# Optimization experiments

Measured on AMD Instinct MI355X. Metric: run time of the kernel, lower is better.

Reference implementation:

```python
import jax, jax.numpy as jnp
import numpy as np
import math

B, T, M, C, H = 2, 2048, 77, 512, 8
D = C // H  # head dim = 64


def setup_inputs() -> dict:
    key = jax.random.key(0)
    ks = jax.random.split(key, 20)
    s = 0.02
    inp = {
        "x": jax.random.normal(ks[0], (B, T, C), jnp.float32),
        "c": jax.random.normal(ks[1], (B, M, C), jnp.float32),
        # causal mask for self-attention (masked_fill where == 0)
        "attn_mask": jnp.tril(jnp.ones((T, T), jnp.int32))[None, None],
        "padding_mask": jnp.ones((B, M), jnp.int32),
    }
    names = ["Wq", "Wk", "Wv", "Wkc", "Wvc", "Wg1", "Wg2", "Wp"]
    for i, n in enumerate(names):
        inp[n] = jax.random.normal(ks[2 + i], (C, C), jnp.float32) * s
        inp["b" + n[1:]] = jnp.zeros((C,), jnp.float32)
    return inp


def _heads(t):
    # [B, S, C] -> [B, S, H, D]
    return t.reshape(t.shape[0], t.shape[1], H, D)


def reference(x, c, attn_mask, padding_mask,
              Wq, bq, Wk, bk, Wv, bv, Wkc, bkc, Wvc, bvc,
              Wg1, bg1, Wg2, bg2, Wp, bp):
    scale = 1.0 / math.sqrt(D)
    q = _heads(x @ Wq + bq)      # [B,T,H,D]
    k = _heads(x @ Wk + bk)      # [B,T,H,D]
    v = _heads(x @ Wv + bv)
    k_c = _heads(c @ Wkc + bkc)  # [B,M,H,D]
    v_c = _heads(c @ Wvc + bvc)

    # self-attention branch
    att = jnp.einsum("bthd,bshd->bhts", q, k) * scale   # [B,H,T,T]
    att = jnp.where(attn_mask == 0, -jnp.inf, att)
    att = jax.nn.softmax(att, axis=-1)
    y = jnp.einsum("bhts,bshd->bthd", att, v).reshape(B, T, C)

    # cross-attention branch to condition c
    att_c = jnp.einsum("bthd,bmhd->bhtm", q, k_c) * scale  # [B,H,T,M]
    att_c = jnp.where(padding_mask[:, None, None, :] == 0, -jnp.inf, att_c)
    att_c = jax.nn.softmax(att_c, axis=-1)
    y_c = jnp.einsum("bhtm,bmhd->bthd", att_c, v_c).reshape(B, T, C)

    # sigmoid gating fusion (note: gates cross-multiply branches, per source)
    gate_self = jax.nn.sigmoid(y @ Wg1 + bg1)
    gate_c = jax.nn.sigmoid(y_c @ Wg2 + bg2)
    y = gate_self * y_c + gate_c * y
    return y @ Wp + bp
```

## Files before the change

### kernel.cpp

```cpp
#include <hip/hip_runtime.h>
#include <hip/hip_bf16.h>
#include <math.h>

#define BB 2
#define TT 2048
#define MM 77
#define CC 512
#define HH 8
#define DD 64

typedef short bf16x8 __attribute__((ext_vector_type(8)));
typedef float f32x4  __attribute__((ext_vector_type(4)));

static __device__ __forceinline__ unsigned short f2bf(float x) {
    __hip_bfloat16 h = __float2bfloat16(x);
    return *reinterpret_cast<unsigned short*>(&h);
}
static __device__ __forceinline__ float bf2f(unsigned short u) {
    unsigned int v = ((unsigned int)u) << 16;
    return *reinterpret_cast<float*>(&v);
}

__global__ __launch_bounds__(256)
void wconv8(const float* __restrict__ w0, const float* __restrict__ w1,
            const float* __restrict__ w2, const float* __restrict__ w3,
            const float* __restrict__ w4, const float* __restrict__ w5,
            const float* __restrict__ w6, const float* __restrict__ w7,
            unsigned short* __restrict__ outbase)
{
    const float* W;
    switch (blockIdx.z) {
        case 0: W = w0; break; case 1: W = w1; break;
        case 2: W = w2; break; case 3: W = w3; break;
        case 4: W = w4; break; case 5: W = w5; break;
        case 6: W = w6; break; default: W = w7; break;
    }
    unsigned short* Wp = outbase + (size_t)blockIdx.z * 512 * 512;
    const int k0 = blockIdx.x * 64;
    const int n0 = blockIdx.y * 64;
    const int tid = threadIdx.x;
    __shared__ unsigned short t[64 * 72];

    #pragma unroll
    for (int it = 0; it < 4; ++it) {
        const int e = tid + 256 * it;
        const int r  = e >> 4;
        const int c4 = (e & 15) * 4;
        const float4 v = *(const float4*)(W + (size_t)(k0 + r) * 512 + n0 + c4);
        t[(c4 + 0) * 72 + r] = f2bf(v.x);
        t[(c4 + 1) * 72 + r] = f2bf(v.y);
        t[(c4 + 2) * 72 + r] = f2bf(v.z);
        t[(c4 + 3) * 72 + r] = f2bf(v.w);
    }
    __syncthreads();
    #pragma unroll
    for (int it = 0; it < 2; ++it) {
        const int e    = tid + 256 * it;
        const int gl   = e >> 7;
        const int ktl  = (e >> 6) & 1;
        const int lane = e & 63;
        const int l15  = lane & 15;
        const int q    = lane >> 4;
        const int4 v = *(const int4*)&t[(gl * 16 + l15) * 72 + ktl * 32 + q * 8];
        const int G  = (n0 >> 4) + gl;
        const int KT = (k0 >> 5) + ktl;
        *(int4*)(Wp + ((size_t)(G * 16 + KT) * 64 + lane) * 8) = v;
    }
}

__global__ __launch_bounds__(256)
void proj_all(const float* __restrict__ x, const float* __restrict__ cin,
              const unsigned short* __restrict__ Wt8,
              const float* __restrict__ bq, const float* __restrict__ bk,
              const float* __restrict__ bv, const float* __restrict__ bkc,
              const float* __restrict__ bvc,
              unsigned short* __restrict__ qb,
              unsigned short* __restrict__ vtb,
              unsigned short* __restrict__ kcb,
              unsigned short* __restrict__ vtcb)
{
    __shared__ unsigned short As[4 * 16 * 64 * 8];

    const int tid = threadIdx.x;
    int b = blockIdx.x;
    const float* Ap; const unsigned short* Wtp;
    const float *bb0, *bb1, *bb2;
    int row0, colb, N, isSelf;
    if (b < 384) {
        isSelf = 1;
        row0 = (b & 63) * 64; colb = (b >> 6) * 256;
        Ap = x; Wtp = Wt8; N = BB * TT;
        bb0 = bq; bb1 = bk; bb2 = bv;
    } else {
        b -= 384; isSelf = 0;
        row0 = (b % 3) * 64; colb = (b / 3) * 256;
        Ap = cin; Wtp = Wt8 + 3 * 262144; N = BB * MM;
        bb0 = bkc; bb1 = bvc; bb2 = nullptr;
    }

    #pragma unroll
    for (int half = 0; half < 2; ++half) {
        const int r    = half * 32 + (tid >> 3);
        const int rg   = r >> 4;
        const int l15r = r & 15;
        const int seg  = (tid & 7) * 64;
        const int gr   = row0 + r;
        unsigned short tmp[64];
        #pragma unroll
        for (int j = 0; j < 16; ++j) {
            float4 v = (gr < N) ? *(const float4*)(Ap + (size_t)gr * 512 + seg + j * 4)
                                : make_float4(0.f, 0.f, 0.f, 0.f);
            tmp[j*4+0] = f2bf(v.x); tmp[j*4+1] = f2bf(v.y);
            tmp[j*4+2] = f2bf(v.z); tmp[j*4+3] = f2bf(v.w);
        }
        #pragma unroll
        for (int jb = 0; jb < 8; ++jb) {
            const int k  = seg + jb * 8;
            const int kt = k >> 5;
            const int q  = (k >> 3) & 3;
            *(int4*)&As[((rg * 16 + kt) * 64 + q * 16 + l15r) * 8] = *(int4*)&tmp[jb*8];
        }
    }
    __syncthreads();

    const int wv   = tid >> 6;
    const int lane = tid & 63;
    const int l15  = lane & 15;
    const int quad = lane >> 4;
    const int wc   = colb + wv * 64;
    const int wcg  = wc >> 4;

    f32x4 acc[4][4];
    #pragma unroll
    for (int mi = 0; mi < 4; ++mi)
        #pragma unroll
        for (int ni = 0; ni < 4; ++ni) acc[mi][ni] = (f32x4){0.f, 0.f, 0.f, 0.f};

    bf16x8 b0v[4], b1v[4], b2v[4];
    #pragma unroll
    for (int ni = 0; ni < 4; ++ni) {
        b0v[ni] = *(const bf16x8*)(Wtp + (((size_t)(wcg + ni) * 16 + 0) << 9) + lane * 8);
        b1v[ni] = *(const bf16x8*)(Wtp + (((size_t)(wcg + ni) * 16 + 1) << 9) + lane * 8);
    }

    for (int kt = 0; kt < 16; ++kt) {
        if (kt + 2 < 16) {
            #pragma unroll
            for (int ni = 0; ni < 4; ++ni)
                b2v[ni] = *(const bf16x8*)(Wtp + (((size_t)(wcg + ni) * 16 + kt + 2) << 9) + lane * 8);
        }
        bf16x8 a[4];
        #pragma unroll
        for (int mi = 0; mi < 4; ++mi)
            a[mi] = *(const bf16x8*)&As[((mi * 16 + kt) * 64 + lane) * 8];
        #pragma unroll
        for (int ni = 0; ni < 4; ++ni)
            #pragma unroll
            for (int mi = 0; mi < 4; ++mi)
                acc[mi][ni] = __builtin_amdgcn_mfma_f32_16x16x32_bf16(a[mi], b0v[ni], acc[mi][ni], 0, 0, 0);
        #pragma unroll
        for (int ni = 0; ni < 4; ++ni) { b0v[ni] = b1v[ni]; b1v[ni] = b2v[ni]; }
    }

    const int which = wc >> 9;
    const float* bsel = (which == 0) ? bb0 : ((which == 1) ? bb1 : bb2);
    const float sc = (isSelf && which == 0) ? 0.125f : 1.f;

    float bvv[4];
    #pragma unroll
    for (int ni = 0; ni < 4; ++ni)
        bvv[ni] = bsel[(wc + ni * 16 + l15) & 511];

    if (isSelf) {
        const int b_ = row0 >> 11;
        const int t0 = row0 & 2047;
        const int h  = (wc & 511) >> 6;
        __syncthreads();
        unsigned short* TL = (unsigned short*)As + wv * (64 * 72);
        if (which < 2) {
            #pragma unroll
            for (int mi = 0; mi < 4; ++mi)
                #pragma unroll
                for (int ni = 0; ni < 4; ++ni)
                    #pragma unroll
                    for (int reg = 0; reg < 4; ++reg) {
                        const int t = mi * 16 + quad * 4 + reg;
                        const int d = ni * 16 + l15;
                        TL[t * 72 + d] = f2bf((acc[mi][ni][reg] + bvv[ni]) * sc);
                    }
            unsigned short* dst = qb + (size_t)which * 2097152
                                + (((size_t)b_ * 8 + h) * 2048 + t0) * 64;
            #pragma unroll
            for (int it = 0; it < 8; ++it) {
                const int t = it * 8 + (lane >> 3);
                *(int4*)(dst + (size_t)t * 64 + (lane & 7) * 8)
                    = *(const int4*)&TL[t * 72 + (lane & 7) * 8];
            }
        } else {
            #pragma unroll
            for (int mi = 0; mi < 4; ++mi)
                #pragma unroll
                for (int ni = 0; ni < 4; ++ni) {
                    ushort4 u;
                    u.x = f2bf(acc[mi][ni][0] + bvv[ni]);
                    u.y = f2bf(acc[mi][ni][1] + bvv[ni]);
                    u.z = f2bf(acc[mi][ni][2] + bvv[ni]);
                    u.w = f2bf(acc[mi][ni][3] + bvv[ni]);
                    const int d = ni * 16 + l15;
                    *(ushort4*)&TL[d * 72 + mi * 16 + quad * 4] = u;
                }
            unsigned short* dst = vtb + (((size_t)b_ * 8 + h) * 64) * 2048 + t0;
            #pragma unroll
            for (int it = 0; it < 8; ++it) {
                const int d = it * 8 + (lane >> 3);
                *(int4*)(dst + (size_t)d * 2048 + (lane & 7) * 8)
                    = *(const int4*)&TL[d * 72 + (lane & 7) * 8];
            }
        }
    } else {
        #pragma unroll
        for (int mi = 0; mi < 4; ++mi)
            #pragma unroll
            for (int reg = 0; reg < 4; ++reg) {
                const int row = row0 + mi * 16 + quad * 4 + reg;
                if (row >= N) continue;
                const int b_ = (row >= MM) ? 1 : 0;
                const int m_ = row - b_ * MM;
                #pragma unroll
                for (int ni = 0; ni < 4; ++ni) {
                    const float v = acc[mi][ni][reg] + bvv[ni];
                    const int cl = (wc + ni * 16 + l15) & 511;
                    const int h = cl >> 6, d = cl & 63;
                    if (which == 0)
                        kcb[(((size_t)b_ * 8 + h) * 77 + m_) * 64 + d] = f2bf(v);
                    else
                        vtcb[(((size_t)b_ * 8 + h) * 64 + d) * 128 + m_] = f2bf(v);
                }
            }
    }
}

template<int ACT, int OUT, int AMODE, int MI>
__global__ __launch_bounds__(256)
void gemm_rs(const void* __restrict__ A0, const void* __restrict__ A1,
             const void* __restrict__ A2, const void* __restrict__ A3,
             const unsigned short* __restrict__ Wt,
             const float* __restrict__ b0, const float* __restrict__ b1,
             void* __restrict__ out0, void* __restrict__ out1,
             int N, int NC)
{
    __shared__ unsigned short As[MI * 16 * 64 * 8];

    const int tid  = threadIdx.x;
    const int z    = blockIdx.z;
    const int row0 = blockIdx.x * (MI * 16);
    const int colb = blockIdx.y * 256;
    const void* Ap = z ? A1 : A0;

    #pragma unroll
    for (int half = 0; half < MI / 2; ++half) {
        const int r    = half * 32 + (tid >> 3);
        const int rg   = r >> 4;
        const int l15r = r & 15;
        const int seg  = (tid & 7) * 64;
        const int gr   = row0 + r;
        unsigned short tmp[64];
        if (AMODE == 2) {
            #pragma unroll
            for (int jb = 0; jb < 8; ++jb) {
                unsigned short a[8], bq_[8], c[8], d[8];
                if (gr < N) {
                    const size_t off = (size_t)gr * 512 + seg + jb * 8;
                    *(int4*)a   = *(const int4*)((const unsigned short*)A0 + off);
                    *(int4*)bq_ = *(const int4*)((const unsigned short*)A1 + off);
                    *(int4*)c   = *(const int4*)((const unsigned short*)A2 + off);
                    *(int4*)d   = *(const int4*)((const unsigned short*)A3 + off);
                    #pragma unroll
                    for (int k = 0; k < 8; ++k)
                        tmp[jb*8+k] = f2bf(bf2f(a[k]) * bf2f(bq_[k]) + bf2f(c[k]) * bf2f(d[k]));
                } else {
                    #pragma unroll
                    for (int k = 0; k < 8; ++k) tmp[jb*8+k] = 0;
                }
            }
        } else {
            const unsigned short* Ab = (const unsigned short*)Ap;
            #pragma unroll
            for (int jb = 0; jb < 8; ++jb) {
                int4 v = (gr < N) ? *(const int4*)(Ab + (size_t)gr * 512 + seg + jb * 8)
                                  : make_int4(0, 0, 0, 0);
                *(int4*)&tmp[jb*8] = v;
            }
        }
        #pragma unroll
        for (int jb = 0; jb < 8; ++jb) {
            const int k  = seg + jb * 8;
            const int kt = k >> 5;
            const int q  = (k >> 3) & 3;
            *(int4*)&As[((rg * 16 + kt) * 64 + q * 16 + l15r) * 8] = *(int4*)&tmp[jb*8];
        }
    }
    __syncthreads();

    const int wv   = tid >> 6;
    const int lane = tid & 63;
    const int l15  = lane & 15;
    const int quad = lane >> 4;
    const int wc   = colb + wv * 64;
    const int wcg  = wc >> 4;

    f32x4 acc[MI][4];
    #pragma unroll
    for (int mi = 0; mi < MI; ++mi)
        #pragma unroll
        for (int ni = 0; ni < 4; ++ni) acc[mi][ni] = (f32x4){0.f, 0.f, 0.f, 0.f};

    const unsigned short* Wz = Wt + (size_t)z * NC;

    bf16x8 b0v[4], b1v[4], b2v[4];
    #pragma unroll
    for (int ni = 0; ni < 4; ++ni) {
        b0v[ni] = *(const bf16x8*)(Wz + (((size_t)(wcg + ni) * 16 + 0) << 9) + lane * 8);
        b1v[ni] = *(const bf16x8*)(Wz + (((size_t)(wcg + ni) * 16 + 1) << 9) + lane * 8);
    }

    for (int kt = 0; kt < 16; ++kt) {
        if (kt + 2 < 16) {
            #pragma unroll
            for (int ni = 0; ni < 4; ++ni)
                b2v[ni] = *(const bf16x8*)(Wz + (((size_t)(wcg + ni) * 16 + kt + 2) << 9) + lane * 8);
        }
        bf16x8 a[MI];
        #pragma unroll
        for (int mi = 0; mi < MI; ++mi)
            a[mi] = *(const bf16x8*)&As[((mi * 16 + kt) * 64 + lane) * 8];
        #pragma unroll
        for (int ni = 0; ni < 4; ++ni)
            #pragma unroll
            for (int mi = 0; mi < MI; ++mi)
                acc[mi][ni] = __builtin_amdgcn_mfma_f32_16x16x32_bf16(a[mi], b0v[ni], acc[mi][ni], 0, 0, 0);
        #pragma unroll
        for (int ni = 0; ni < 4; ++ni) { b0v[ni] = b1v[ni]; b1v[ni] = b2v[ni]; }
    }

    const float* bsel = ((OUT == 1) && z) ? b1 : b0;
    float bvv[4];
    #pragma unroll
    for (int ni = 0; ni < 4; ++ni)
        bvv[ni] = bsel[(wc + ni * 16 + l15) & 511];

    #pragma unroll
    for (int mi = 0; mi < MI; ++mi) {
        #pragma unroll
        for (int reg = 0; reg < 4; ++reg) {
            const int row = row0 + mi * 16 + quad * 4 + reg;
            if (row >= N) continue;
            #pragma unroll
            for (int ni = 0; ni < 4; ++ni) {
                float v = acc[mi][ni][reg] + bvv[ni];
                if (ACT == 1) v = 1.f / (1.f + __expf(-v));
                const int col = wc + ni * 16 + l15;
                if (OUT == 0) {
                    ((float*)out0)[(size_t)row * 512 + col] = v;
                } else {
                    unsigned short* dst = (unsigned short*)(z ? out1 : out0);
                    dst[(size_t)row * 512 + col] = f2bf(v);
                }
            }
        }
    }
}

__global__ __launch_bounds__(256)
void attn_all(const unsigned short* __restrict__ Qh,
              const unsigned short* __restrict__ Kh,
              const unsigned short* __restrict__ Vth,
              unsigned short* __restrict__ yout,
              const unsigned short* __restrict__ Kch,
              const unsigned short* __restrict__ Vtch,
              unsigned short* __restrict__ ycout)
{
    int lin = blockIdx.x;
    int causal, S_kv, W, bh, qt;
    const unsigned short *Kb, *Vb;
    unsigned short* outp;
    if (lin < 512) {
        causal = 1; S_kv = TT; W = TT;
        bh = (lin & 7) | (((lin >> 3) & 1) << 3);
        const int qtr = lin >> 4;
        qt = (qtr < 16) ? (31 - qtr) : (qtr - 16);
        Kb = Kh + (size_t)bh * S_kv * 64;
        Vb = Vth + (size_t)bh * 64 * W;
        outp = yout;
    } else {
        lin -= 512;
        causal = 0; S_kv = MM; W = 128;
        bh = (lin & 7) | (((lin >> 3) & 1) << 3);
        qt = lin >> 4;
        Kb = Kch + (size_t)bh * S_kv * 64;
        Vb = Vtch + (size_t)bh * 64 * W;
        outp = ycout;
    }
    const int n_kt = causal ? (qt + 1) : 2;
    const int vlim = causal ? TT : MM;

    const int tid  = threadIdx.x;
    const int wv   = tid >> 6;
    const int lane = tid & 63;
    const int l15  = lane & 15;
    const int quad = lane >> 4;

    __shared__ unsigned short Ks[2][64 * 80];
    __shared__ unsigned short Vs[2][64 * 80];
    __shared__ unsigned short PT[4 * 16 * 72];

    const int t0 = qt * 64 + wv * 16;
    const unsigned short* qptr = Qh + ((size_t)bh * TT + t0 + l15) * 64 + quad * 8;
    const bf16x8 qb0 = *(const bf16x8*)(qptr);
    const bf16x8 qb1 = *(const bf16x8*)(qptr + 32);

    f32x4 Oacc[4];
    #pragma unroll
    for (int dt = 0; dt < 4; ++dt) Oacc[dt] = (f32x4){0.f, 0.f, 0.f, 0.f};
    float l = 0.f;

    int4 kR[2], vR[2];
    {
        #pragma unroll
        for (int it = 0; it < 2; ++it) {
            const int e = tid + 256 * it;
            const int row = e >> 3, blk = e & 7;
            kR[it] = (row < S_kv)
                ? *(const int4*)(Kb + (size_t)row * 64 + blk * 8) : make_int4(0,0,0,0);
            vR[it] = (blk * 8 < W)
                ? *(const int4*)(Vb + (size_t)row * W + blk * 8) : make_int4(0,0,0,0);
        }
        #pragma unroll
        for (int it = 0; it < 2; ++it) {
            const int e = tid + 256 * it;
            const int row = e >> 3, blk = e & 7;
            *(int4*)&Ks[0][row * 80 + ((blk ^ (row & 7)) * 8)] = kR[it];
            *(int4*)&Vs[0][row * 80 + ((blk ^ (row & 7)) * 8)] = vR[it];
        }
    }
    __syncthreads();

    for (int kt = 0; kt < n_kt; ++kt) {
        const int buf = kt & 1;
        const int s0 = kt * 64;

        if (kt + 1 < n_kt) {
            const int s1 = (kt + 1) * 64;
            #pragma unroll
            for (int it = 0; it < 2; ++it) {
                const int e = tid + 256 * it;
                const int row = e >> 3, blk = e & 7;
                const int s = s1 + row;
                kR[it] = (s < S_kv)
                    ? *(const int4*)(Kb + (size_t)s * 64 + blk * 8) : make_int4(0,0,0,0);
                const int c0 = s1 + blk * 8;
                int4 vv = make_int4(0, 0, 0, 0);
                if (c0 < vlim) {
                    vv = *(const int4*)(Vb + (size_t)row * W + c0);
                    if (c0 + 8 > vlim) {
                        unsigned short* sp = (unsigned short*)&vv;
                        #pragma unroll
                        for (int j = 0; j < 8; ++j)
                            if (c0 + j >= vlim) sp[j] = 0;
                    }
                }
                vR[it] = vv;
            }
        }

        f32x4 sacc[4];
        #pragma unroll
        for (int mt = 0; mt < 4; ++mt) {
            const int krow = 16 * mt + l15;
            const bf16x8 ka0 = *(const bf16x8*)&Ks[buf][krow * 80 + (((quad    ) ^ (krow & 7)) * 8)];
            const bf16x8 ka1 = *(const bf16x8*)&Ks[buf][krow * 80 + (((quad + 4) ^ (krow & 7)) * 8)];
            sacc[mt] = (f32x4){0.f, 0.f, 0.f, 0.f};
            sacc[mt] = __builtin_amdgcn_mfma_f32_16x16x32_bf16(ka0, qb0, sacc[mt], 0, 0, 0);
            sacc[mt] = __builtin_amdgcn_mfma_f32_16x16x32_bf16(ka1, qb1, sacc[mt], 0, 0, 0);
        }

        float sv[16];
        #pragma unroll
        for (int mt = 0; mt < 4; ++mt)
            #pragma unroll
            for (int reg = 0; reg < 4; ++reg)
                sv[mt * 4 + reg] = sacc[mt][reg];

        const bool cmask = (causal && kt == qt);
        if (cmask || (s0 + 64 > S_kv)) {
            const int lim = cmask ? (t0 + l15) : 0x7fffffff;
            #pragma unroll
            for (int mt = 0; mt < 4; ++mt)
                #pragma unroll
                for (int reg = 0; reg < 4; ++reg) {
                    const int kg = s0 + 16 * mt + quad * 4 + reg;
                    if (kg > lim || kg >= S_kv) sv[mt * 4 + reg] = -INFINITY;
                }
        }

        float p[16], psum = 0.f;
        #pragma unroll
        for (int i = 0; i < 16; ++i) { p[i] = __expf(sv[i]); psum += p[i]; }
        psum += __shfl_xor(psum, 16);
        psum += __shfl_xor(psum, 32);
        l += psum;

        unsigned short* ptw = &PT[wv * 16 * 72 + l15 * 72];
        #pragma unroll
        for (int mt = 0; mt < 4; ++mt) {
            ushort4 u;
            u.x = f2bf(p[mt * 4 + 0]); u.y = f2bf(p[mt * 4 + 1]);
            u.z = f2bf(p[mt * 4 + 2]); u.w = f2bf(p[mt * 4 + 3]);
            *(ushort4*)(ptw + 16 * mt + quad * 4) = u;
        }
        const bf16x8 pb0 = *(const bf16x8*)(ptw + quad * 8);
        const bf16x8 pb1 = *(const bf16x8*)(ptw + quad * 8 + 32);

        #pragma unroll
        for (int dt = 0; dt < 4; ++dt) {
            const int vrow = 16 * dt + l15;
            const bf16x8 va0 = *(const bf16x8*)&Vs[buf][vrow * 80 + (((quad    ) ^ (vrow & 7)) * 8)];
            const bf16x8 va1 = *(const bf16x8*)&Vs[buf][vrow * 80 + (((quad + 4) ^ (vrow & 7)) * 8)];
            Oacc[dt] = __builtin_amdgcn_mfma_f32_16x16x32_bf16(va0, pb0, Oacc[dt], 0, 0, 0);
            Oacc[dt] = __builtin_amdgcn_mfma_f32_16x16x32_bf16(va1, pb1, Oacc[dt], 0, 0, 0);
        }

        if (kt + 1 < n_kt) {
            const int nbuf = buf ^ 1;
            #pragma unroll
            for (int it = 0; it < 2; ++it) {
                const int e = tid + 256 * it;
                const int row = e >> 3, blk = e & 7;
                *(int4*)&Ks[nbuf][row * 80 + ((blk ^ (row & 7)) * 8)] = kR[it];
                *(int4*)&Vs[nbuf][row * 80 + ((blk ^ (row & 7)) * 8)] = vR[it];
            }
        }
        __syncthreads();
    }

    const int b = bh >> 3, h = bh & 7;
    const float inv_l = 1.f / l;
    const int t = t0 + l15;
    unsigned short* ob = outp + ((size_t)b * TT + t) * CC + h * DD + quad * 4;
    #pragma unroll
    for (int dt = 0; dt < 4; ++dt) {
        ushort4 u;
        u.x = f2bf(Oacc[dt][0] * inv_l);
        u.y = f2bf(Oacc[dt][1] * inv_l);
        u.z = f2bf(Oacc[dt][2] * inv_l);
        u.w = f2bf(Oacc[dt][3] * inv_l);
        *(ushort4*)(ob + 16 * dt) = u;
    }
}

extern "C" void kernel_launch(void* const* d_in, const int* in_sizes, int n_in,
                              void* d_out, int out_size, void* d_ws, size_t ws_size,
                              hipStream_t stream)
{
    const float* x   = (const float*)d_in[0];
    const float* cin = (const float*)d_in[1];
    const float* Wq  = (const float*)d_in[4];   const float* bq  = (const float*)d_in[5];
    const float* Wk  = (const float*)d_in[6];   const float* bk  = (const float*)d_in[7];
    const float* Wv  = (const float*)d_in[8];   const float* bv  = (const float*)d_in[9];
    const float* Wkc = (const float*)d_in[10];  const float* bkc = (const float*)d_in[11];
    const float* Wvc = (const float*)d_in[12];  const float* bvc = (const float*)d_in[13];
    const float* Wg1 = (const float*)d_in[14];  const float* bg1 = (const float*)d_in[15];
    const float* Wg2 = (const float*)d_in[16];  const float* bg2 = (const float*)d_in[17];
    const float* Wp  = (const float*)d_in[18];  const float* bp  = (const float*)d_in[19];

    float* out = (float*)d_out;
    char*  w   = (char*)d_ws;
    const size_t MB = 1024 * 1024;

    unsigned short* Wt8  = (unsigned short*)(w);
    unsigned short* qb   = (unsigned short*)(w + 4  * MB);
    unsigned short* vtb  = (unsigned short*)(w + 12 * MB);
    unsigned short* yb   = (unsigned short*)(w + 20 * MB);
    unsigned short* ycb  = (unsigned short*)(w + 24 * MB);
    unsigned short* g1b  = (unsigned short*)(w + 28 * MB);
    unsigned short* g2b  = (unsigned short*)(w + 32 * MB);
    unsigned short* kcb  = (unsigned short*)(w + 40 * MB);
    unsigned short* vtcb = (unsigned short*)(w + 40 * MB + 256 * 1024);

    const dim3 blk(256);

    wconv8<<<dim3(8, 8, 8), blk, 0, stream>>>(Wq, Wk, Wv, Wkc, Wvc, Wg1, Wg2, Wp, Wt8);

    proj_all<<<dim3(396), blk, 0, stream>>>(
        x, cin, Wt8, bq, bk, bv, bkc, bvc, qb, vtb, kcb, vtcb);

    attn_all<<<dim3(1024), blk, 0, stream>>>(
        qb, qb + 2097152, vtb, yb, kcb, vtcb, ycb);

    gemm_rs<1, 1, 0, 4><<<dim3(64, 2, 2), blk, 0, stream>>>(
        yb, ycb, nullptr, nullptr, Wt8 + 5 * 262144, bg1, bg2, g1b, g2b,
        BB * TT, 262144);

    gemm_rs<0, 0, 2, 2><<<dim3(128, 2), blk, 0, stream>>>(
        g1b, ycb, g2b, yb, Wt8 + 7 * 262144, bp, nullptr, out, nullptr,
        BB * TT, 0);
}
```

Baseline: 224.5 us.

## Load K/V fragments directly from global memory in attention, dropping LDS staging

The attention kernel no longer stages K and V tiles through double-buffered shared memory with block-wide barriers. Each wave now loads its MFMA operand fragments straight from global memory, relying on L1/L2 reuse across the four waves. To keep the cross-attention V padding safe, the producer GEMM zero-fills V^T columns 77..127. It also adds s_setprio around the MFMA blocks. This removes the LDS writes and __syncthreads, but each wave now re-reads K/V from global memory and loses the explicit prefetch overlap.

```diff
diff --git a/kernel.cpp b/kernel.cpp
--- a/kernel.cpp
+++ b/kernel.cpp
@@ -237,6 +237,19 @@
                         vtcb[(((size_t)b_ * 8 + h) * 64 + d) * 128 + m_] = f2bf(v);
                 }
             }
+        if (which == 1 && row0 == 128) {
+            const int h0 = (colb - 512) >> 6;
+            for (int e = tid; e < 2 * 4 * 64; e += 256) {
+                const int d  = e & 63;
+                const int hl = (e >> 6) & 3;
+                const int bz = e >> 8;
+                unsigned short* rp = vtcb + (((size_t)bz * 8 + h0 + hl) * 64 + d) * 128;
+                rp[77] = 0; rp[78] = 0; rp[79] = 0;
+                #pragma unroll
+                for (int q8 = 80; q8 < 128; q8 += 8)
+                    *(int4*)(rp + q8) = make_int4(0, 0, 0, 0);
+            }
+        }
     }
 }
 
@@ -402,7 +415,6 @@
         outp = ycout;
     }
     const int n_kt = causal ? (qt + 1) : 2;
-    const int vlim = causal ? TT : MM;
 
     const int tid  = threadIdx.x;
     const int wv   = tid >> 6;
@@ -410,8 +422,6 @@
     const int l15  = lane & 15;
     const int quad = lane >> 4;
 
-    __shared__ unsigned short Ks[2][64 * 80];
-    __shared__ unsigned short Vs[2][64 * 80];
     __shared__ unsigned short PT[4 * 16 * 72];
 
     const int t0 = qt * 64 + wv * 16;
@@ -424,65 +434,35 @@
     for (int dt = 0; dt < 4; ++dt) Oacc[dt] = (f32x4){0.f, 0.f, 0.f, 0.f};
     float l = 0.f;
 
-    int4 kR[2], vR[2];
-    {
-        #pragma unroll
-        for (int it = 0; it < 2; ++it) {
-            const int e = tid + 256 * it;
-            const int row = e >> 3, blk = e & 7;
-            kR[it] = (row < S_kv)
-                ? *(const int4*)(Kb + (size_t)row * 64 + blk * 8) : make_int4(0,0,0,0);
-            vR[it] = (blk * 8 < W)
-                ? *(const int4*)(Vb + (size_t)row * W + blk * 8) : make_int4(0,0,0,0);
-        }
-        #pragma unroll
-        for (int it = 0; it < 2; ++it) {
-            const int e = tid + 256 * it;
-            const int row = e >> 3, blk = e & 7;
-            *(int4*)&Ks[0][row * 80 + ((blk ^ (row & 7)) * 8)] = kR[it];
-            *(int4*)&Vs[0][row * 80 + ((blk ^ (row & 7)) * 8)] = vR[it];
-        }
-    }
-    __syncthreads();
+    const unsigned short* kbase = Kb + (size_t)l15 * 64 + quad * 8;
+    const unsigned short* vbase = Vb + (size_t)l15 * W + quad * 8;
 
     for (int kt = 0; kt < n_kt; ++kt) {
-        const int buf = kt & 1;
         const int s0 = kt * 64;
 
-        if (kt + 1 < n_kt) {
-            const int s1 = (kt + 1) * 64;
-            #pragma unroll
-            for (int it = 0; it < 2; ++it) {
-                const int e = tid + 256 * it;
-                const int row = e >> 3, blk = e & 7;
-                const int s = s1 + row;
-                kR[it] = (s < S_kv)
-                    ? *(const int4*)(Kb + (size_t)s * 64 + blk * 8) : make_int4(0,0,0,0);
-                const int c0 = s1 + blk * 8;
-                int4 vv = make_int4(0, 0, 0, 0);
-                if (c0 < vlim) {
-                    vv = *(const int4*)(Vb + (size_t)row * W + c0);
-                    if (c0 + 8 > vlim) {
-                        unsigned short* sp = (unsigned short*)&vv;
-                        #pragma unroll
-                        for (int j = 0; j < 8; ++j)
-                            if (c0 + j >= vlim) sp[j] = 0;
-                    }
-                }
-                vR[it] = vv;
-            }
+        bf16x8 ka0[4], ka1[4], va0[4], va1[4];
+        #pragma unroll
+        for (int mt = 0; mt < 4; ++mt) {
+            const unsigned short* kp = kbase + (size_t)(s0 + 16 * mt) * 64;
+            ka0[mt] = *(const bf16x8*)(kp);
+            ka1[mt] = *(const bf16x8*)(kp + 32);
+        }
+        #pragma unroll
+        for (int dt = 0; dt < 4; ++dt) {
+            const unsigned short* vp = vbase + (size_t)(16 * dt) * W + s0;
+            va0[dt] = *(const bf16x8*)(vp);
+            va1[dt] = *(const bf16x8*)(vp + 32);
         }
 
         f32x4 sacc[4];
+        __builtin_amdgcn_s_setprio(1);
         #pragma unroll
         for (int mt = 0; mt < 4; ++mt) {
-            const int krow = 16 * mt + l15;
-            const bf16x8 ka0 = *(const bf16x8*)&Ks[buf][krow * 80 + (((quad    ) ^ (krow & 7)) * 8)];
-            const bf16x8 ka1 = *(const bf16x8*)&Ks[buf][krow * 80 + (((quad + 4) ^ (krow & 7)) * 8)];
             sacc[mt] = (f32x4){0.f, 0.f, 0.f, 0.f};
-            sacc[mt] = __builtin_amdgcn_mfma_f32_16x16x32_bf16(ka0, qb0, sacc[mt], 0, 0, 0);
-            sacc[mt] = __builtin_amdgcn_mfma_f32_16x16x32_bf16(ka1, qb1, sacc[mt], 0, 0, 0);
-        }
+            sacc[mt] = __builtin_amdgcn_mfma_f32_16x16x32_bf16(ka0[mt], qb0, sacc[mt], 0, 0, 0);
+            sacc[mt] = __builtin_amdgcn_mfma_f32_16x16x32_bf16(ka1[mt], qb1, sacc[mt], 0, 0, 0);
+        }
+        __builtin_amdgcn_s_setprio(0);
 
         float sv[16];
         #pragma unroll
@@ -521,26 +501,13 @@
         const bf16x8 pb0 = *(const bf16x8*)(ptw + quad * 8);
         const bf16x8 pb1 = *(const bf16x8*)(ptw + quad * 8 + 32);
 
+        __builtin_amdgcn_s_setprio(1);
         #pragma unroll
         for (int dt = 0; dt < 4; ++dt) {
-            const int vrow = 16 * dt + l15;
-            const bf16x8 va0 = *(const bf16x8*)&Vs[buf][vrow * 80 + (((quad    ) ^ (vrow & 7)) * 8)];
-            const bf16x8 va1 = *(const bf16x8*)&Vs[buf][vrow * 80 + (((quad + 4) ^ (vrow & 7)) * 8)];
-            Oacc[dt] = __builtin_amdgcn_mfma_f32_16x16x32_bf16(va0, pb0, Oacc[dt], 0, 0, 0);
-            Oacc[dt] = __builtin_amdgcn_mfma_f32_16x16x32_bf16(va1, pb1, Oacc[dt], 0, 0, 0);
-        }
-
-        if (kt + 1 < n_kt) {
-            const int nbuf = buf ^ 1;
-            #pragma unroll
-            for (int it = 0; it < 2; ++it) {
-                const int e = tid + 256 * it;
-                const int row = e >> 3, blk = e & 7;
-                *(int4*)&Ks[nbuf][row * 80 + ((blk ^ (row & 7)) * 8)] = kR[it];
-                *(int4*)&Vs[nbuf][row * 80 + ((blk ^ (row & 7)) * 8)] = vR[it];
-            }
-        }
-        __syncthreads();
+            Oacc[dt] = __builtin_amdgcn_mfma_f32_16x16x32_bf16(va0[dt], pb0, Oacc[dt], 0, 0, 0);
+            Oacc[dt] = __builtin_amdgcn_mfma_f32_16x16x32_bf16(va1[dt], pb1, Oacc[dt], 0, 0, 0);
+        }
+        __builtin_amdgcn_s_setprio(0);
     }
 
     const int b = bh >> 3, h = bh & 7;
```

Measured after the change: 240.8 us. 7.2% more time.
